# Optimization experiments

Measured on AMD Instinct MI355X. Metric: run time of the kernel, lower is better.

The kernel has to match this reference:

```python
import jax, jax.numpy as jnp
import numpy as np
import math

B, T, C = 2, 2048, 2048
H, G, HS = 16, 4, 128  # n_head, n_query_groups, head_size
EPS = 1e-5
SCALE = 1.0 / math.sqrt(HS)
QKV_DIM = (H + 2 * G) * HS  # 3072, gate logits (H) appended after


def _build_rope(seq_len, n_elem, base):
    freq = base ** (np.arange(0, n_elem, 2, dtype=np.float64) / n_elem)
    inv_freq = 1.0 / freq
    idx_theta = np.outer(np.arange(seq_len, dtype=np.float64), inv_freq)
    return (jnp.asarray(np.cos(idx_theta), dtype=jnp.float32),
            jnp.asarray(np.sin(idx_theta), dtype=jnp.float32))


def setup_inputs() -> dict:
    key = jax.random.key(0)
    k1, k2, k3 = jax.random.split(key, 3)
    x = jax.random.normal(k1, (B, T, C), dtype=jnp.float32)
    # rope base per module: 0.09 * local_window ** 1.628
    base = 0.09 * (2048.0 ** 1.628)
    cos, sin = _build_rope(T, HS, base)  # [T, HS//2]
    W_attn = jax.random.normal(k2, (QKV_DIM + H, C), dtype=jnp.float32) * 0.02
    W_proj = jax.random.normal(k3, (C, H * HS), dtype=jnp.float32) * 0.02
    q_norm_w = jnp.ones((HS,), dtype=jnp.float32)
    k_norm_w = jnp.ones((HS,), dtype=jnp.float32)
    return {"x": x, "cos": cos, "sin": sin, "W_attn": W_attn,
            "q_norm_w": q_norm_w, "k_norm_w": k_norm_w, "W_proj": W_proj}


def _rms_norm(v, w):
    # per-head RMSNorm over last dim (head_size)
    ms = jnp.mean(jnp.square(v), axis=-1, keepdims=True)
    return v * jax.lax.rsqrt(ms + EPS) * w


def _apply_rope(v, cos, sin):
    # v: [B, T, N, HS]; cos/sin: [T, HS//2]; non-interleaved halves
    d2 = v.shape[-1] // 2
    x1, x2 = v[..., :d2], v[..., d2:]
    c = cos[None, :, None, :]
    s = sin[None, :, None, :]
    return jnp.concatenate([x1 * c - x2 * s, x2 * c + x1 * s], axis=-1)


def reference(x, cos, sin, W_attn, q_norm_w, k_norm_w, W_proj):
    qkv = jnp.einsum('btc,oc->bto', x, W_attn)  # [B, T, QKV_DIM+H]
    q = qkv[..., : H * HS].reshape(B, T, H, HS)
    k = qkv[..., H * HS:(H + G) * HS].reshape(B, T, G, HS)
    v = qkv[..., (H + G) * HS: QKV_DIM].reshape(B, T, G, HS)
    gate = qkv[..., QKV_DIM:]  # [B, T, H]

    q = _apply_rope(_rms_norm(q, q_norm_w), cos, sin)
    k = _apply_rope(_rms_norm(k, k_norm_w), cos, sin)

    rep = H // G
    kr = jnp.repeat(k, rep, axis=2)  # [B, T, H, HS]
    vr = jnp.repeat(v, rep, axis=2)

    scores = jnp.einsum('bthd,bshd->bhts', q, kr) * SCALE  # [B, H, T, T]
    causal = jnp.tril(jnp.ones((T, T), dtype=bool))
    scores = jnp.where(causal, scores, jnp.finfo(scores.dtype).min)
    probs = jax.nn.softmax(scores, axis=-1)
    out = jnp.einsum('bhts,bshd->bthd', probs, vr)  # [B, T, H, HS]

    out = out * jax.nn.sigmoid(gate)[..., None]  # gated attention, per-head
    y = jnp.einsum('bto,co->btc', out.reshape(B, T, H * HS), W_proj)
    return y
```

## Files before the change

### kernel.cpp

```cpp
#include <hip/hip_runtime.h>

#define T_   2048
#define BB   2
#define CC   2048
#define HH   16
#define GG   4
#define HSS  128
#define QKVD 3072
#define NQKV 3088
#define NPAD 3200
#define SCALE_ 0.08838834764831845f
#define SCALE2_ (0.08838834764831845f * 1.4426950408889634f)

typedef __attribute__((ext_vector_type(8))) short  short8;
typedef __attribute__((ext_vector_type(4))) float  f32x4;
typedef __attribute__((ext_vector_type(4))) int    v4i;
typedef __attribute__((ext_vector_type(4))) float  v4f;
typedef __attribute__((ext_vector_type(4))) unsigned short u16x4;

typedef const void __attribute__((address_space(1)))* gas1_t;
typedef void __attribute__((address_space(3)))* as3_t;

__device__ __forceinline__ void gl_lds16(const void* g, void* l) {
    __builtin_amdgcn_global_load_lds((gas1_t)g, (as3_t)l, 16, 0, 0);
}

__device__ __forceinline__ unsigned short f2bf(float f) {
    unsigned u = __float_as_uint(f);
    u += 0x7fffu + ((u >> 16) & 1u);
    return (unsigned short)(u >> 16);
}
__device__ __forceinline__ unsigned short f2bf_fast(float f) {
    return (unsigned short)((__float_as_uint(f) + 0x8000u) >> 16);
}
__device__ __forceinline__ float bf2f(unsigned short h) {
    return __uint_as_float(((unsigned)h) << 16);
}

template <int CTRL>
__device__ __forceinline__ float dppmv(float x) {
    int i = __float_as_int(x);
    return __int_as_float(__builtin_amdgcn_update_dpp(i, i, CTRL, 0xF, 0xF, false));
}
__device__ __forceinline__ void red16_max(float* v) {
#pragma unroll
    for (int r = 0; r < 4; ++r) v[r] = fmaxf(v[r], dppmv<0xB1>(v[r]));
#pragma unroll
    for (int r = 0; r < 4; ++r) v[r] = fmaxf(v[r], dppmv<0x4E>(v[r]));
#pragma unroll
    for (int r = 0; r < 4; ++r) v[r] = fmaxf(v[r], dppmv<0x124>(v[r]));
#pragma unroll
    for (int r = 0; r < 4; ++r) v[r] = fmaxf(v[r], dppmv<0x128>(v[r]));
}
__device__ __forceinline__ void red16_sum(float* v) {
#pragma unroll
    for (int r = 0; r < 4; ++r) v[r] += dppmv<0xB1>(v[r]);
#pragma unroll
    for (int r = 0; r < 4; ++r) v[r] += dppmv<0x4E>(v[r]);
#pragma unroll
    for (int r = 0; r < 4; ++r) v[r] += dppmv<0x124>(v[r]);
#pragma unroll
    for (int r = 0; r < 4; ++r) v[r] += dppmv<0x128>(v[r]);
}

__global__ void k_convert3(const float* __restrict__ x, const float* __restrict__ wa,
                           const float* __restrict__ wp,
                           unsigned short* __restrict__ xb, unsigned short* __restrict__ wab,
                           unsigned short* __restrict__ wpb) {
    const int id = blockIdx.x;
    const float* src; unsigned short* dst; int base, n_src4;
    if (id < 8192)       { src = x;  dst = xb;  base = id;         n_src4 = 2097152; }
    else if (id < 14592) { src = wa; dst = wab; base = id - 8192;  n_src4 = 1581056; }
    else                 { src = wp; dst = wpb; base = id - 14592; n_src4 = 1048576; }
    int i = base * 256 + threadIdx.x;
    u16x4 o;
    if (i < n_src4) {
        v4f v = *(const v4f*)(src + (size_t)i * 4);
        o[0] = f2bf(v[0]); o[1] = f2bf(v[1]); o[2] = f2bf(v[2]); o[3] = f2bf(v[3]);
    } else {
        o[0] = 0; o[1] = 0; o[2] = 0; o[3] = 0;
    }
    *(u16x4*)(dst + (size_t)i * 4) = o;
}

template <int BM_, typename OutT>
__launch_bounds__(512, 2)
__global__ void k_gemm8(const unsigned short* __restrict__ A,
                        const unsigned short* __restrict__ Bm,
                        OutT* __restrict__ C,
                        int K, int lda, int ldb, int ldc, int nmax) {
    constexpr int MI  = BM_ / 32;
    constexpr int NPH = MI / 2;
    __shared__ unsigned short As[2][BM_ * 64];
    __shared__ unsigned short Bs[2][256 * 64];
    const int t = threadIdx.x;
    const int lane = t & 63;
    const int wid  = t >> 6;
    const int wr = wid >> 2, wc = wid & 3;
    const int bm = blockIdx.x, bn = blockIdx.y;
    const int fro = lane & 15, fk = lane >> 4;

    const int srow  = lane >> 3;
    const size_t scol = (size_t)(((lane & 7) ^ srow) * 8);

    const unsigned short* Abase = A  + (size_t)(bm * BM_) * lda;
    const unsigned short* Bbase = Bm + (size_t)(bn * 256) * ldb;

    f32x4 acc[MI][4];
#pragma unroll
    for (int i = 0; i < MI; ++i)
#pragma unroll
        for (int j = 0; j < 4; ++j) acc[i][j] = (f32x4){0.f, 0.f, 0.f, 0.f};

#pragma unroll
    for (int h = 0; h < 2; ++h)
#pragma unroll
        for (int c8 = 0; c8 < 2; ++c8) {
            const int rr = h * 128 + wid * 16 + c8 * 8;
            if (BM_ == 256 || h == 0)
                gl_lds16(Abase + (size_t)(rr + srow) * lda + scol, &As[0][rr * 64]);
            gl_lds16(Bbase + (size_t)(rr + srow) * ldb + scol, &Bs[0][rr * 64]);
        }

    int cur = 0;
    for (int kt = 0; kt < K; kt += 64) {
        asm volatile("s_waitcnt vmcnt(0)" ::: "memory");
        __builtin_amdgcn_s_barrier();
        __builtin_amdgcn_sched_barrier(0);
        const bool pf = (kt + 64 < K);
        const int nxt = cur ^ 1;
        const int kn = kt + 64;

        short8 bf_[4][2];
#pragma unroll
        for (int q = 0; q < NPH; ++q) {
            short8 af[2][2];
#pragma unroll
            for (int im = 0; im < 2; ++im)
#pragma unroll
                for (int kk = 0; kk < 2; ++kk) {
                    const int ar = wr * (BM_ / 2) + (q * 2 + im) * 16 + fro;
                    af[im][kk] = *(const short8*)&As[cur][ar * 64 + ((kk * 4 + fk) ^ (ar & 7)) * 8];
                }
            if (q == 0) {
#pragma unroll
                for (int ni = 0; ni < 4; ++ni)
#pragma unroll
                    for (int kk = 0; kk < 2; ++kk) {
                        const int br = wc * 64 + ni * 16 + fro;
                        bf_[ni][kk] = *(const short8*)&Bs[cur][br * 64 + ((kk * 4 + fk) ^ (br & 7)) * 8];
                    }
            }
            if (pf) {
                if (BM_ == 256) {
                    const int h = q & 1;
#pragma unroll
                    for (int c8 = 0; c8 < 2; ++c8) {
                        const int rr = h * 128 + wid * 16 + c8 * 8;
                        if ((q >> 1) == 0)
                            gl_lds16(Abase + (size_t)(rr + srow) * lda + kn + scol, &As[nxt][rr * 64]);
                        else
                            gl_lds16(Bbase + (size_t)(rr + srow) * ldb + kn + scol, &Bs[nxt][rr * 64]);
                    }
                } else {
                    if (q == 0) {
#pragma unroll
                        for (int c8 = 0; c8 < 2; ++c8) {
                            const int rr = wid * 16 + c8 * 8;
                            gl_lds16(Abase + (size_t)(rr + srow) * lda + kn + scol, &As[nxt][rr * 64]);
                        }
                    } else {
#pragma unroll
                        for (int h = 0; h < 2; ++h)
#pragma unroll
                            for (int c8 = 0; c8 < 2; ++c8) {
                                const int rr = h * 128 + wid * 16 + c8 * 8;
                                gl_lds16(Bbase + (size_t)(rr + srow) * ldb + kn + scol, &Bs[nxt][rr * 64]);
                            }
                    }
                }
            }
            __builtin_amdgcn_s_setprio(1);
#pragma unroll
            for (int im = 0; im < 2; ++im)
#pragma unroll
                for (int ni = 0; ni < 4; ++ni)
#pragma unroll
                    for (int kk = 0; kk < 2; ++kk)
                        acc[q * 2 + im][ni] = __builtin_amdgcn_mfma_f32_16x16x32_bf16(
                            af[im][kk], bf_[ni][kk], acc[q * 2 + im][ni], 0, 0, 0);
            __builtin_amdgcn_s_setprio(0);
            __builtin_amdgcn_s_barrier();
        }
        cur ^= 1;
    }

    const int col16 = lane & 15, rbase = (lane >> 4) * 4;
    const int gr0 = bm * BM_ + wr * (BM_ / 2);
    const int gc0 = bn * 256 + wc * 64;
#pragma unroll
    for (int mi = 0; mi < MI; ++mi)
#pragma unroll
        for (int ni = 0; ni < 4; ++ni) {
            const int gcol = gc0 + ni * 16 + col16;
            if (gcol < nmax) {
#pragma unroll
                for (int r = 0; r < 4; ++r) {
                    const int grow = gr0 + mi * 16 + rbase + r;
                    float v = acc[mi][ni][r];
                    if constexpr (sizeof(OutT) == 2)
                        C[(size_t)grow * ldc + gcol] = (OutT)f2bf(v);
                    else
                        C[(size_t)grow * ldc + gcol] = (OutT)v;
                }
            }
        }
}

__global__ void k_normtrans(unsigned short* __restrict__ qkv,
                            const float* __restrict__ cosT, const float* __restrict__ sinT,
                            const float* __restrict__ qw, const float* __restrict__ kw,
                            unsigned short* __restrict__ vt) {
    __shared__ unsigned short tile[64][65];
    const int id = blockIdx.x;
    if (id < 20480) {
        const int lane = threadIdx.x & 63;
        const int row  = id * 4 + (threadIdx.x >> 6);
        const int tok  = row / 20;
        const int hh   = row - tok * 20;
        const int tpos = tok & (T_ - 1);
        unsigned short* rp = qkv + (size_t)tok * NPAD + (hh < 16 ? hh * 128 : 2048 + (hh - 16) * 128);
        const float* w = (hh < 16) ? qw : kw;
        const float sc_ = (hh < 16) ? SCALE2_ : 1.0f;
        float e1 = bf2f(rp[lane]);
        float e2 = bf2f(rp[lane + 64]);
        float ss = e1 * e1 + e2 * e2;
#pragma unroll
        for (int m = 1; m < 64; m <<= 1) ss += __shfl_xor(ss, m);
        float inv = rsqrtf(ss * (1.0f / 128.0f) + 1e-5f);
        float n1 = e1 * inv * w[lane];
        float n2 = e2 * inv * w[lane + 64];
        float c = cosT[tpos * 64 + lane];
        float s = sinT[tpos * 64 + lane];
        rp[lane]      = f2bf((n1 * c - n2 * s) * sc_);
        rp[lane + 64] = f2bf((n2 * c + n1 * s) * sc_);
    } else {
        const int t2 = id - 20480;
        const int b = (t2 & 7) >> 2, g = t2 & 3;
        const int s0 = ((t2 >> 3) & 31) * 64, d0 = (t2 >> 8) * 64;
        const int tx = threadIdx.x & 63, ty0 = threadIdx.x >> 6;
        const unsigned short* src = qkv + (size_t)(b * T_ + s0) * NPAD + 2560 + g * 128 + d0;
#pragma unroll
        for (int r = 0; r < 16; ++r) {
            int ty = ty0 * 16 + r;
            tile[ty][tx] = src[(size_t)ty * NPAD + tx];
        }
        __syncthreads();
        unsigned short* dstp = vt + ((size_t)(b * GG + g) * 128 + d0) * T_ + s0;
#pragma unroll
        for (int r = 0; r < 16; ++r) {
            int ty = ty0 * 16 + r;
            dstp[(size_t)ty * T_ + tx] = tile[tx][ty];
        }
    }
}

__launch_bounds__(512, 4)
__global__ void k_attn(const unsigned short* __restrict__ qkv,
                       const unsigned short* __restrict__ vt,
                       unsigned short* __restrict__ ao) {
    __shared__ unsigned short Ks[64 * 128];
    __shared__ unsigned short Vs[128 * 64];
    __shared__ unsigned short Ps[8][16 * 64];
    const int t = threadIdx.x;
    const int lane = t & 63;
    const int wid  = t >> 6;
    const int id = blockIdx.x;
    const int bg = id & 7;
    const int hh = (id >> 3) & 3;
    const int prx = (id >> 5) & 7;
    const int pr = (id & 256) ? (15 - prx) : prx;
    const int b = bg >> 2, g = bg & 3, h = g * 4 + hh;
    const int fro = lane & 15, fk = lane >> 4;
    const int rbase = fk * 4;

    const int qt  = (wid < 4) ? pr : 31 - pr;
    const int wq  = wid & 3;
    const int q0w = qt * 64 + wq * 16;
    const int nt_own  = qt + 1;
    const int nt_loop = 32 - pr;

    const unsigned short* kg0 = qkv + (size_t)(b * T_) * NPAD + 2048 + g * 128;
    const unsigned short* vg0 = vt + (size_t)(b * GG + g) * 128 * T_;

    short8 qf[4];
    const unsigned short* qp = qkv + (size_t)(b * T_ + q0w + fro) * NPAD + h * 128 + fk * 8;
#pragma unroll
    for (int kb = 0; kb < 4; ++kb) qf[kb] = *(const short8*)(qp + kb * 32);

    float m_r[4], l_r[4];
    f32x4 o[8];
#pragma unroll
    for (int r = 0; r < 4; ++r) { m_r[r] = -1e30f; l_r[r] = 0.f; }
#pragma unroll
    for (int d = 0; d < 8; ++d) o[d] = (f32x4){0.f, 0.f, 0.f, 0.f};

    const int cp0 = wid * 2;

    for (int ti = 0; ti < nt_loop; ++ti) {
        const int s0 = ti * 64;
        __syncthreads();
#pragma unroll
        for (int p = 0; p < 2; ++p) {
            const int cp = cp0 + p;
            const int kr = cp * 4 + (lane >> 4);
            const int sK = lane & 15;
            gl_lds16(kg0 + (size_t)(s0 + kr) * NPAD + (size_t)((sK ^ (kr & 7)) * 8), &Ks[cp * 512]);
            const int d  = cp * 8 + (lane >> 3);
            const int sV = lane & 7;
            gl_lds16(vg0 + (size_t)d * T_ + s0 + (size_t)((sV ^ (d & 7)) * 8), &Vs[cp * 512]);
        }
        __syncthreads();

        if (ti < nt_own) {
            f32x4 sc[4];
#pragma unroll
            for (int jb = 0; jb < 4; ++jb) sc[jb] = (f32x4){0.f, 0.f, 0.f, 0.f};
#pragma unroll
            for (int jb = 0; jb < 4; ++jb) {
                const int kr = jb * 16 + fro;
#pragma unroll
                for (int kb = 0; kb < 4; ++kb) {
                    short8 kf = *(const short8*)&Ks[kr * 128 + 8 * ((kb * 4 + fk) ^ (kr & 7))];
                    sc[jb] = __builtin_amdgcn_mfma_f32_16x16x32_bf16(qf[kb], kf, sc[jb], 0, 0, 0);
                }
            }
            if (ti == qt) {
#pragma unroll
                for (int jb = 0; jb < 4; ++jb)
#pragma unroll
                    for (int r = 0; r < 4; ++r)
                        if ((jb * 16 + fro) > (wq * 16 + rbase + r)) sc[jb][r] = -1e30f;
            }
            float mx[4], rs[4];
#pragma unroll
            for (int r = 0; r < 4; ++r)
                mx[r] = fmaxf(fmaxf(sc[0][r], sc[1][r]), fmaxf(sc[2][r], sc[3][r]));
            red16_max(mx);
            bool grow = false;
#pragma unroll
            for (int r = 0; r < 4; ++r) grow = grow || (mx[r] > m_r[r] + 8.f);
            if (__any(grow ? 1 : 0)) {
#pragma unroll
                for (int r = 0; r < 4; ++r) {
                    float mn = fmaxf(m_r[r], mx[r]);
                    float fs = exp2f(m_r[r] - mn);
                    m_r[r] = mn;
                    l_r[r] *= fs;
#pragma unroll
                    for (int d = 0; d < 8; ++d) o[d][r] *= fs;
                }
            }
#pragma unroll
            for (int jb = 0; jb < 4; ++jb)
#pragma unroll
                for (int r = 0; r < 4; ++r) sc[jb][r] = exp2f(sc[jb][r] - m_r[r]);
#pragma unroll
            for (int r = 0; r < 4; ++r)
                rs[r] = (sc[0][r] + sc[1][r]) + (sc[2][r] + sc[3][r]);
            red16_sum(rs);
#pragma unroll
            for (int r = 0; r < 4; ++r) l_r[r] += rs[r];
            unsigned short* pw = &Ps[wid][0];
#pragma unroll
            for (int jb = 0; jb < 4; ++jb)
#pragma unroll
                for (int r = 0; r < 4; ++r) {
                    const int row = rbase + r;
                    const int slot = jb * 2 + (fro >> 3);
                    pw[row * 64 + ((slot ^ (row & 7)) * 8 + (fro & 7))] = f2bf_fast(sc[jb][r]);
                }
            asm volatile("s_waitcnt lgkmcnt(0)" ::: "memory");
            __builtin_amdgcn_sched_barrier(0);
            short8 pa[2];
#pragma unroll
            for (int ks = 0; ks < 2; ++ks)
                pa[ks] = *(const short8*)&Ps[wid][fro * 64 + ((ks * 4 + fk) ^ (fro & 7)) * 8];
#pragma unroll
            for (int ks = 0; ks < 2; ++ks)
#pragma unroll
                for (int db = 0; db < 8; ++db) {
                    const int d = db * 16 + fro;
                    short8 vf = *(const short8*)&Vs[d * 64 + 8 * ((ks * 4 + fk) ^ (d & 7))];
                    o[db] = __builtin_amdgcn_mfma_f32_16x16x32_bf16(pa[ks], vf, o[db], 0, 0, 0);
                }
        }
    }
#pragma unroll
    for (int r = 0; r < 4; ++r) {
        const int qrow = q0w + rbase + r;
        float gv = bf2f(qkv[(size_t)(b * T_ + qrow) * NPAD + QKVD + h]);
        float sg = 1.f / (1.f + __expf(-gv));
        float invl = sg / l_r[r];
        unsigned short* orow = ao + (size_t)(b * T_ + qrow) * 2048 + h * 128;
#pragma unroll
        for (int db = 0; db < 8; ++db)
            orow[db * 16 + fro] = f2bf(o[db][r] * invl);
    }
}

extern "C" void kernel_launch(void* const* d_in, const int* in_sizes, int n_in,
                              void* d_out, int out_size, void* d_ws, size_t ws_size,
                              hipStream_t stream) {
    const float* x      = (const float*)d_in[0];
    const float* cosT   = (const float*)d_in[1];
    const float* sinT   = (const float*)d_in[2];
    const float* W_attn = (const float*)d_in[3];
    const float* qw     = (const float*)d_in[4];
    const float* kw     = (const float*)d_in[5];
    const float* W_proj = (const float*)d_in[6];

    char* ws = (char*)d_ws;
    const size_t OFF_XB   = 0;
    const size_t OFF_WAB  = 16777216;
    const size_t OFF_WPB  = 29884416;
    const size_t OFF_QKV  = 38273024;
    const size_t OFF_VT   = 64487424;
    const size_t OFF_AO   = 68681728;
    const size_t NEED     = 85458944;
    if (ws_size < NEED) return;

    unsigned short* xb   = (unsigned short*)(ws + OFF_XB);
    unsigned short* wab  = (unsigned short*)(ws + OFF_WAB);
    unsigned short* wpb  = (unsigned short*)(ws + OFF_WPB);
    unsigned short* qkvb = (unsigned short*)(ws + OFF_QKV);
    unsigned short* vtb  = (unsigned short*)(ws + OFF_VT);
    unsigned short* aob  = (unsigned short*)(ws + OFF_AO);

    k_convert3<<<18688, 256, 0, stream>>>(x, W_attn, W_proj, xb, wab, wpb);
    k_gemm8<256, unsigned short><<<dim3(16, 13), 512, 0, stream>>>(xb, wab, qkvb, 2048, 2048, 2048, NPAD, NPAD);
    k_normtrans<<<20992, 256, 0, stream>>>(qkvb, cosT, sinT, qw, kw, vtb);
    k_attn<<<512, 512, 0, stream>>>(qkvb, vtb, aob);
    k_gemm8<128, float><<<dim3(32, 8), 512, 0, stream>>>(aob, wpb, (float*)d_out, 2048, 2048, 2048, 2048, 2048);
}
```

Baseline: 211.2 us.

## Split long causal query tile across both wave groups with split-K merge

Reworks the attention work split so that, once the short query tile finishes, wave group A takes half of the KV range of the long query tile while group B handles the other half. The two partial softmax states are merged through LDS before the gated epilogue. This balances per-wave work inside each block, so the short-tile waves no longer sit idle at barriers while the long tile runs. The cost is a second K/V LDS buffer (raising LDS use, which may limit occupancy), extra staging traffic per iteration and a merge step at the end.

Result: slower. 221.6 us (+4.9%).

```diff
diff --git a/kernel.cpp b/kernel.cpp
--- a/kernel.cpp
+++ b/kernel.cpp
@@ -269,8 +269,10 @@
 __global__ void k_attn(const unsigned short* __restrict__ qkv,
                        const unsigned short* __restrict__ vt,
                        unsigned short* __restrict__ ao) {
-    __shared__ unsigned short Ks[64 * 128];
-    __shared__ unsigned short Vs[128 * 64];
+    __shared__ unsigned short KsB[64 * 128];
+    __shared__ unsigned short VsB[128 * 64];
+    __shared__ unsigned short KsA[64 * 128];
+    __shared__ unsigned short VsA[128 * 64];
     __shared__ unsigned short Ps[8][16 * 64];
     const int t = threadIdx.x;
     const int lane = t & 63;
@@ -283,20 +285,13 @@
     const int b = bg >> 2, g = bg & 3, h = g * 4 + hh;
     const int fro = lane & 15, fk = lane >> 4;
     const int rbase = fk * 4;
-
-    const int qt  = (wid < 4) ? pr : 31 - pr;
-    const int wq  = wid & 3;
-    const int q0w = qt * 64 + wq * 16;
-    const int nt_own  = qt + 1;
-    const int nt_loop = 32 - pr;
+    const bool grpA = (wid < 4);
+    const int wq = wid & 3;
+    const int qtB = 31 - pr;
 
     const unsigned short* kg0 = qkv + (size_t)(b * T_) * NPAD + 2048 + g * 128;
     const unsigned short* vg0 = vt + (size_t)(b * GG + g) * 128 * T_;
-
-    short8 qf[4];
-    const unsigned short* qp = qkv + (size_t)(b * T_ + q0w + fro) * NPAD + h * 128 + fk * 8;
-#pragma unroll
-    for (int kb = 0; kb < 4; ++kb) qf[kb] = *(const short8*)(qp + kb * 32);
+    const int cp0 = wid * 2;
 
     float m_r[4], l_r[4];
     f32x4 o[8];
@@ -305,107 +300,176 @@
 #pragma unroll
     for (int d = 0; d < 8; ++d) o[d] = (f32x4){0.f, 0.f, 0.f, 0.f};
 
-    const int cp0 = wid * 2;
-
-    for (int ti = 0; ti < nt_loop; ++ti) {
-        const int s0 = ti * 64;
-        __syncthreads();
+    short8 qf[4];
+    {
+        const int q0 = (grpA ? pr : qtB) * 64 + wq * 16;
+        const unsigned short* qp = qkv + (size_t)(b * T_ + q0 + fro) * NPAD + h * 128 + fk * 8;
+#pragma unroll
+        for (int kb = 0; kb < 4; ++kb) qf[kb] = *(const short8*)(qp + kb * 32);
+    }
+
+    auto stage_pair = [&](unsigned short* Kd, unsigned short* Vd, int tile) {
+        const int s0 = tile * 64;
 #pragma unroll
         for (int p = 0; p < 2; ++p) {
             const int cp = cp0 + p;
             const int kr = cp * 4 + (lane >> 4);
             const int sK = lane & 15;
-            gl_lds16(kg0 + (size_t)(s0 + kr) * NPAD + (size_t)((sK ^ (kr & 7)) * 8), &Ks[cp * 512]);
+            gl_lds16(kg0 + (size_t)(s0 + kr) * NPAD + (size_t)((sK ^ (kr & 7)) * 8), &Kd[cp * 512]);
             const int d  = cp * 8 + (lane >> 3);
             const int sV = lane & 7;
-            gl_lds16(vg0 + (size_t)d * T_ + s0 + (size_t)((sV ^ (d & 7)) * 8), &Vs[cp * 512]);
-        }
+            gl_lds16(vg0 + (size_t)d * T_ + s0 + (size_t)((sV ^ (d & 7)) * 8), &Vd[cp * 512]);
+        }
+    };
+
+    auto compute_tile = [&](const unsigned short* Kb, const unsigned short* Vb, bool domask) {
+        f32x4 sc[4];
+#pragma unroll
+        for (int jb = 0; jb < 4; ++jb) sc[jb] = (f32x4){0.f, 0.f, 0.f, 0.f};
+#pragma unroll
+        for (int jb = 0; jb < 4; ++jb) {
+            const int kr = jb * 16 + fro;
+#pragma unroll
+            for (int kb = 0; kb < 4; ++kb) {
+                short8 kf = *(const short8*)&Kb[kr * 128 + 8 * ((kb * 4 + fk) ^ (kr & 7))];
+                sc[jb] = __builtin_amdgcn_mfma_f32_16x16x32_bf16(qf[kb], kf, sc[jb], 0, 0, 0);
+            }
+        }
+        if (domask) {
+#pragma unroll
+            for (int jb = 0; jb < 4; ++jb)
+#pragma unroll
+                for (int r = 0; r < 4; ++r)
+                    if ((jb * 16 + fro) > (wq * 16 + rbase + r)) sc[jb][r] = -1e30f;
+        }
+        float mx[4], rs[4];
+#pragma unroll
+        for (int r = 0; r < 4; ++r)
+            mx[r] = fmaxf(fmaxf(sc[0][r], sc[1][r]), fmaxf(sc[2][r], sc[3][r]));
+        red16_max(mx);
+        bool growb = false;
+#pragma unroll
+        for (int r = 0; r < 4; ++r) growb = growb || (mx[r] > m_r[r] + 8.f);
+        if (__any(growb ? 1 : 0)) {
+#pragma unroll
+            for (int r = 0; r < 4; ++r) {
+                float mn = fmaxf(m_r[r], mx[r]);
+                float fs = exp2f(m_r[r] - mn);
+                m_r[r] = mn;
+                l_r[r] *= fs;
+#pragma unroll
+                for (int d = 0; d < 8; ++d) o[d][r] *= fs;
+            }
+        }
+#pragma unroll
+        for (int jb = 0; jb < 4; ++jb)
+#pragma unroll
+            for (int r = 0; r < 4; ++r) sc[jb][r] = exp2f(sc[jb][r] - m_r[r]);
+#pragma unroll
+        for (int r = 0; r < 4; ++r)
+            rs[r] = (sc[0][r] + sc[1][r]) + (sc[2][r] + sc[3][r]);
+        red16_sum(rs);
+#pragma unroll
+        for (int r = 0; r < 4; ++r) l_r[r] += rs[r];
+        unsigned short* pw = &Ps[wid][0];
+#pragma unroll
+        for (int jb = 0; jb < 4; ++jb)
+#pragma unroll
+            for (int r = 0; r < 4; ++r) {
+                const int row = rbase + r;
+                const int slot = jb * 2 + (fro >> 3);
+                pw[row * 64 + ((slot ^ (row & 7)) * 8 + (fro & 7))] = f2bf_fast(sc[jb][r]);
+            }
+        asm volatile("s_waitcnt lgkmcnt(0)" ::: "memory");
+        __builtin_amdgcn_sched_barrier(0);
+        short8 pa[2];
+#pragma unroll
+        for (int ks = 0; ks < 2; ++ks)
+            pa[ks] = *(const short8*)&Ps[wid][fro * 64 + ((ks * 4 + fk) ^ (fro & 7)) * 8];
+#pragma unroll
+        for (int ks = 0; ks < 2; ++ks)
+#pragma unroll
+            for (int db = 0; db < 8; ++db) {
+                const int d = db * 16 + fro;
+                short8 vf = *(const short8*)&Vb[d * 64 + 8 * ((ks * 4 + fk) ^ (d & 7))];
+                o[db] = __builtin_amdgcn_mfma_f32_16x16x32_bf16(pa[ks], vf, o[db], 0, 0, 0);
+            }
+    };
+
+    auto epilogue = [&](int q0e) {
+#pragma unroll
+        for (int r = 0; r < 4; ++r) {
+            const int qrow = q0e + rbase + r;
+            float gv = bf2f(qkv[(size_t)(b * T_ + qrow) * NPAD + QKVD + h]);
+            float sg = 1.f / (1.f + __expf(-gv));
+            float invl = sg / l_r[r];
+            unsigned short* orow = ao + (size_t)(b * T_ + qrow) * 2048 + h * 128;
+#pragma unroll
+            for (int db = 0; db < 8; ++db)
+                orow[db * 16 + fro] = f2bf(o[db][r] * invl);
+        }
+    };
+
+    for (int s = 0; s <= pr; ++s) {
         __syncthreads();
-
-        if (ti < nt_own) {
-            f32x4 sc[4];
-#pragma unroll
-            for (int jb = 0; jb < 4; ++jb) sc[jb] = (f32x4){0.f, 0.f, 0.f, 0.f};
-#pragma unroll
-            for (int jb = 0; jb < 4; ++jb) {
-                const int kr = jb * 16 + fro;
-#pragma unroll
-                for (int kb = 0; kb < 4; ++kb) {
-                    short8 kf = *(const short8*)&Ks[kr * 128 + 8 * ((kb * 4 + fk) ^ (kr & 7))];
-                    sc[jb] = __builtin_amdgcn_mfma_f32_16x16x32_bf16(qf[kb], kf, sc[jb], 0, 0, 0);
-                }
-            }
-            if (ti == qt) {
-#pragma unroll
-                for (int jb = 0; jb < 4; ++jb)
-#pragma unroll
-                    for (int r = 0; r < 4; ++r)
-                        if ((jb * 16 + fro) > (wq * 16 + rbase + r)) sc[jb][r] = -1e30f;
-            }
-            float mx[4], rs[4];
-#pragma unroll
-            for (int r = 0; r < 4; ++r)
-                mx[r] = fmaxf(fmaxf(sc[0][r], sc[1][r]), fmaxf(sc[2][r], sc[3][r]));
-            red16_max(mx);
-            bool grow = false;
-#pragma unroll
-            for (int r = 0; r < 4; ++r) grow = grow || (mx[r] > m_r[r] + 8.f);
-            if (__any(grow ? 1 : 0)) {
-#pragma unroll
-                for (int r = 0; r < 4; ++r) {
-                    float mn = fmaxf(m_r[r], mx[r]);
-                    float fs = exp2f(m_r[r] - mn);
-                    m_r[r] = mn;
-                    l_r[r] *= fs;
-#pragma unroll
-                    for (int d = 0; d < 8; ++d) o[d][r] *= fs;
-                }
-            }
-#pragma unroll
-            for (int jb = 0; jb < 4; ++jb)
-#pragma unroll
-                for (int r = 0; r < 4; ++r) sc[jb][r] = exp2f(sc[jb][r] - m_r[r]);
-#pragma unroll
-            for (int r = 0; r < 4; ++r)
-                rs[r] = (sc[0][r] + sc[1][r]) + (sc[2][r] + sc[3][r]);
-            red16_sum(rs);
-#pragma unroll
-            for (int r = 0; r < 4; ++r) l_r[r] += rs[r];
-            unsigned short* pw = &Ps[wid][0];
-#pragma unroll
-            for (int jb = 0; jb < 4; ++jb)
-#pragma unroll
-                for (int r = 0; r < 4; ++r) {
-                    const int row = rbase + r;
-                    const int slot = jb * 2 + (fro >> 3);
-                    pw[row * 64 + ((slot ^ (row & 7)) * 8 + (fro & 7))] = f2bf_fast(sc[jb][r]);
-                }
-            asm volatile("s_waitcnt lgkmcnt(0)" ::: "memory");
-            __builtin_amdgcn_sched_barrier(0);
-            short8 pa[2];
-#pragma unroll
-            for (int ks = 0; ks < 2; ++ks)
-                pa[ks] = *(const short8*)&Ps[wid][fro * 64 + ((ks * 4 + fk) ^ (fro & 7)) * 8];
-#pragma unroll
-            for (int ks = 0; ks < 2; ++ks)
-#pragma unroll
-                for (int db = 0; db < 8; ++db) {
-                    const int d = db * 16 + fro;
-                    short8 vf = *(const short8*)&Vs[d * 64 + 8 * ((ks * 4 + fk) ^ (d & 7))];
-                    o[db] = __builtin_amdgcn_mfma_f32_16x16x32_bf16(pa[ks], vf, o[db], 0, 0, 0);
-                }
-        }
-    }
-#pragma unroll
-    for (int r = 0; r < 4; ++r) {
-        const int qrow = q0w + rbase + r;
-        float gv = bf2f(qkv[(size_t)(b * T_ + qrow) * NPAD + QKVD + h]);
-        float sg = 1.f / (1.f + __expf(-gv));
-        float invl = sg / l_r[r];
-        unsigned short* orow = ao + (size_t)(b * T_ + qrow) * 2048 + h * 128;
-#pragma unroll
-        for (int db = 0; db < 8; ++db)
-            orow[db * 16 + fro] = f2bf(o[db][r] * invl);
+        stage_pair(KsB, VsB, s);
+        __syncthreads();
+        compute_tile(KsB, VsB, grpA && (s == pr));
+    }
+
+    if (grpA) {
+        epilogue(pr * 64 + wq * 16);
+#pragma unroll
+        for (int r = 0; r < 4; ++r) { m_r[r] = -1e30f; l_r[r] = 0.f; }
+#pragma unroll
+        for (int d = 0; d < 8; ++d) o[d] = (f32x4){0.f, 0.f, 0.f, 0.f};
+        const int q0 = qtB * 64 + wq * 16;
+        const unsigned short* qp = qkv + (size_t)(b * T_ + q0 + fro) * NPAD + h * 128 + fk * 8;
+#pragma unroll
+        for (int kb = 0; kb < 4; ++kb) qf[kb] = *(const short8*)(qp + kb * 32);
+    }
+
+    for (int s = pr + 1; s <= 16; ++s) {
+        __syncthreads();
+        stage_pair(KsB, VsB, s);
+        if (s <= 15) stage_pair(KsA, VsA, s + 16 - pr);
+        __syncthreads();
+        if (!grpA)
+            compute_tile(KsB, VsB, (s == 16) && (pr == 15));
+        else if (s <= 15)
+            compute_tile(KsA, VsA, (s == 15) && (pr < 15));
+    }
+
+    __syncthreads();
+    const int ww = wid & 3;
+    unsigned short* obase = (ww & 2) ? VsB : KsB;
+    float* ob = (float*)(obase + (ww & 1) * 4096);
+    float* ml = (float*)KsA + ww * 512;
+    if (grpA) {
+#pragma unroll
+        for (int d = 0; d < 8; ++d) *(f32x4*)&ob[lane * 32 + d * 4] = o[d];
+#pragma unroll
+        for (int r = 0; r < 4; ++r) { ml[lane * 8 + r] = m_r[r]; ml[lane * 8 + 4 + r] = l_r[r]; }
+    }
+    __syncthreads();
+    if (!grpA) {
+        float sB[4], sA[4];
+#pragma unroll
+        for (int r = 0; r < 4; ++r) {
+            float mA = ml[lane * 8 + r];
+            float lA = ml[lane * 8 + 4 + r];
+            float mn = fmaxf(m_r[r], mA);
+            sB[r] = exp2f(m_r[r] - mn);
+            sA[r] = exp2f(mA - mn);
+            l_r[r] = l_r[r] * sB[r] + lA * sA[r];
+        }
+#pragma unroll
+        for (int d = 0; d < 8; ++d) {
+            f32x4 oA = *(const f32x4*)&ob[lane * 32 + d * 4];
+#pragma unroll
+            for (int r = 0; r < 4; ++r) o[d][r] = o[d][r] * sB[r] + oA[r] * sA[r];
+        }
+        epilogue(qtB * 64 + wq * 16);
     }
 }
 
```

## Give each attention wave 32 query rows so K/V fragments feed two MFMAs

Applied to the files above, without the earlier changes.

The attention kernel now runs 4 waves (256 threads) per block instead of 8, and each wave owns 32 query rows as two 16-row sub-tiles. Each K and V fragment read from LDS feeds two MFMAs, which halves LDS read traffic per FLOP and halves the per-block wave count. In exchange, each wave needs roughly twice the registers for accumulators and softmax state. The launch bounds drop to 3 blocks per CU, so fewer waves are resident to hide latency.

New measurement: 315.7 us. 49.4% more time.

```diff
diff --git a/kernel.cpp b/kernel.cpp
--- a/kernel.cpp
+++ b/kernel.cpp
@@ -42,25 +42,27 @@
     int i = __float_as_int(x);
     return __int_as_float(__builtin_amdgcn_update_dpp(i, i, CTRL, 0xF, 0xF, false));
 }
-__device__ __forceinline__ void red16_max(float* v) {
-#pragma unroll
-    for (int r = 0; r < 4; ++r) v[r] = fmaxf(v[r], dppmv<0xB1>(v[r]));
-#pragma unroll
-    for (int r = 0; r < 4; ++r) v[r] = fmaxf(v[r], dppmv<0x4E>(v[r]));
-#pragma unroll
-    for (int r = 0; r < 4; ++r) v[r] = fmaxf(v[r], dppmv<0x124>(v[r]));
-#pragma unroll
-    for (int r = 0; r < 4; ++r) v[r] = fmaxf(v[r], dppmv<0x128>(v[r]));
-}
-__device__ __forceinline__ void red16_sum(float* v) {
-#pragma unroll
-    for (int r = 0; r < 4; ++r) v[r] += dppmv<0xB1>(v[r]);
-#pragma unroll
-    for (int r = 0; r < 4; ++r) v[r] += dppmv<0x4E>(v[r]);
-#pragma unroll
-    for (int r = 0; r < 4; ++r) v[r] += dppmv<0x124>(v[r]);
-#pragma unroll
-    for (int r = 0; r < 4; ++r) v[r] += dppmv<0x128>(v[r]);
+template <int N>
+__device__ __forceinline__ void red16_maxN(float* v) {
+#pragma unroll
+    for (int r = 0; r < N; ++r) v[r] = fmaxf(v[r], dppmv<0xB1>(v[r]));
+#pragma unroll
+    for (int r = 0; r < N; ++r) v[r] = fmaxf(v[r], dppmv<0x4E>(v[r]));
+#pragma unroll
+    for (int r = 0; r < N; ++r) v[r] = fmaxf(v[r], dppmv<0x124>(v[r]));
+#pragma unroll
+    for (int r = 0; r < N; ++r) v[r] = fmaxf(v[r], dppmv<0x128>(v[r]));
+}
+template <int N>
+__device__ __forceinline__ void red16_sumN(float* v) {
+#pragma unroll
+    for (int r = 0; r < N; ++r) v[r] += dppmv<0xB1>(v[r]);
+#pragma unroll
+    for (int r = 0; r < N; ++r) v[r] += dppmv<0x4E>(v[r]);
+#pragma unroll
+    for (int r = 0; r < N; ++r) v[r] += dppmv<0x124>(v[r]);
+#pragma unroll
+    for (int r = 0; r < N; ++r) v[r] += dppmv<0x128>(v[r]);
 }
 
 __global__ void k_convert3(const float* __restrict__ x, const float* __restrict__ wa,
@@ -265,13 +267,13 @@
     }
 }
 
-__launch_bounds__(512, 4)
+__launch_bounds__(256, 3)
 __global__ void k_attn(const unsigned short* __restrict__ qkv,
                        const unsigned short* __restrict__ vt,
                        unsigned short* __restrict__ ao) {
     __shared__ unsigned short Ks[64 * 128];
     __shared__ unsigned short Vs[128 * 64];
-    __shared__ unsigned short Ps[8][16 * 64];
+    __shared__ unsigned short Ps[4][32 * 64];
     const int t = threadIdx.x;
     const int lane = t & 63;
     const int wid  = t >> 6;
@@ -284,34 +286,42 @@
     const int fro = lane & 15, fk = lane >> 4;
     const int rbase = fk * 4;
 
-    const int qt  = (wid < 4) ? pr : 31 - pr;
-    const int wq  = wid & 3;
-    const int q0w = qt * 64 + wq * 16;
+    const bool grpA = (wid < 2);
+    const int wq2 = wid & 1;
+    const int qt  = grpA ? pr : 31 - pr;
+    const int q0w = qt * 64 + wq2 * 32;
     const int nt_own  = qt + 1;
     const int nt_loop = 32 - pr;
 
     const unsigned short* kg0 = qkv + (size_t)(b * T_) * NPAD + 2048 + g * 128;
     const unsigned short* vg0 = vt + (size_t)(b * GG + g) * 128 * T_;
 
-    short8 qf[4];
-    const unsigned short* qp = qkv + (size_t)(b * T_ + q0w + fro) * NPAD + h * 128 + fk * 8;
-#pragma unroll
-    for (int kb = 0; kb < 4; ++kb) qf[kb] = *(const short8*)(qp + kb * 32);
-
-    float m_r[4], l_r[4];
-    f32x4 o[8];
-#pragma unroll
-    for (int r = 0; r < 4; ++r) { m_r[r] = -1e30f; l_r[r] = 0.f; }
-#pragma unroll
-    for (int d = 0; d < 8; ++d) o[d] = (f32x4){0.f, 0.f, 0.f, 0.f};
-
-    const int cp0 = wid * 2;
+    short8 qf[2][4];
+#pragma unroll
+    for (int i = 0; i < 2; ++i) {
+        const unsigned short* qp = qkv + (size_t)(b * T_ + q0w + i * 16 + fro) * NPAD + h * 128 + fk * 8;
+#pragma unroll
+        for (int kb = 0; kb < 4; ++kb) qf[i][kb] = *(const short8*)(qp + kb * 32);
+    }
+
+    float m_r[2][4], l_r[2][4];
+    f32x4 o[2][8];
+#pragma unroll
+    for (int i = 0; i < 2; ++i)
+#pragma unroll
+        for (int r = 0; r < 4; ++r) { m_r[i][r] = -1e30f; l_r[i][r] = 0.f; }
+#pragma unroll
+    for (int i = 0; i < 2; ++i)
+#pragma unroll
+        for (int d = 0; d < 8; ++d) o[i][d] = (f32x4){0.f, 0.f, 0.f, 0.f};
+
+    const int cp0 = wid * 4;
 
     for (int ti = 0; ti < nt_loop; ++ti) {
         const int s0 = ti * 64;
         __syncthreads();
 #pragma unroll
-        for (int p = 0; p < 2; ++p) {
+        for (int p = 0; p < 4; ++p) {
             const int cp = cp0 + p;
             const int kr = cp * 4 + (lane >> 4);
             const int sK = lane & 15;
@@ -323,90 +333,116 @@
         __syncthreads();
 
         if (ti < nt_own) {
-            f32x4 sc[4];
-#pragma unroll
-            for (int jb = 0; jb < 4; ++jb) sc[jb] = (f32x4){0.f, 0.f, 0.f, 0.f};
+            f32x4 sc[2][4];
+#pragma unroll
+            for (int i = 0; i < 2; ++i)
+#pragma unroll
+                for (int jb = 0; jb < 4; ++jb) sc[i][jb] = (f32x4){0.f, 0.f, 0.f, 0.f};
 #pragma unroll
             for (int jb = 0; jb < 4; ++jb) {
                 const int kr = jb * 16 + fro;
 #pragma unroll
                 for (int kb = 0; kb < 4; ++kb) {
                     short8 kf = *(const short8*)&Ks[kr * 128 + 8 * ((kb * 4 + fk) ^ (kr & 7))];
-                    sc[jb] = __builtin_amdgcn_mfma_f32_16x16x32_bf16(qf[kb], kf, sc[jb], 0, 0, 0);
+#pragma unroll
+                    for (int i = 0; i < 2; ++i)
+                        sc[i][jb] = __builtin_amdgcn_mfma_f32_16x16x32_bf16(qf[i][kb], kf, sc[i][jb], 0, 0, 0);
                 }
             }
             if (ti == qt) {
 #pragma unroll
+                for (int i = 0; i < 2; ++i)
+#pragma unroll
+                    for (int jb = 0; jb < 4; ++jb)
+#pragma unroll
+                        for (int r = 0; r < 4; ++r)
+                            if ((jb * 16 + fro) > (wq2 * 32 + i * 16 + rbase + r)) sc[i][jb][r] = -1e30f;
+            }
+            float mx[8], rs[8];
+#pragma unroll
+            for (int i = 0; i < 2; ++i)
+#pragma unroll
+                for (int r = 0; r < 4; ++r)
+                    mx[i * 4 + r] = fmaxf(fmaxf(sc[i][0][r], sc[i][1][r]), fmaxf(sc[i][2][r], sc[i][3][r]));
+            red16_maxN<8>(mx);
+            bool grow = false;
+#pragma unroll
+            for (int i = 0; i < 2; ++i)
+#pragma unroll
+                for (int r = 0; r < 4; ++r) grow = grow || (mx[i * 4 + r] > m_r[i][r] + 8.f);
+            if (__any(grow ? 1 : 0)) {
+#pragma unroll
+                for (int i = 0; i < 2; ++i)
+#pragma unroll
+                    for (int r = 0; r < 4; ++r) {
+                        float mn = fmaxf(m_r[i][r], mx[i * 4 + r]);
+                        float fs = exp2f(m_r[i][r] - mn);
+                        m_r[i][r] = mn;
+                        l_r[i][r] *= fs;
+#pragma unroll
+                        for (int d = 0; d < 8; ++d) o[i][d][r] *= fs;
+                    }
+            }
+#pragma unroll
+            for (int i = 0; i < 2; ++i)
+#pragma unroll
                 for (int jb = 0; jb < 4; ++jb)
 #pragma unroll
-                    for (int r = 0; r < 4; ++r)
-                        if ((jb * 16 + fro) > (wq * 16 + rbase + r)) sc[jb][r] = -1e30f;
-            }
-            float mx[4], rs[4];
-#pragma unroll
-            for (int r = 0; r < 4; ++r)
-                mx[r] = fmaxf(fmaxf(sc[0][r], sc[1][r]), fmaxf(sc[2][r], sc[3][r]));
-            red16_max(mx);
-            bool grow = false;
-#pragma unroll
-            for (int r = 0; r < 4; ++r) grow = grow || (mx[r] > m_r[r] + 8.f);
-            if (__any(grow ? 1 : 0)) {
-#pragma unroll
-                for (int r = 0; r < 4; ++r) {
-                    float mn = fmaxf(m_r[r], mx[r]);
-                    float fs = exp2f(m_r[r] - mn);
-                    m_r[r] = mn;
-                    l_r[r] *= fs;
-#pragma unroll
-                    for (int d = 0; d < 8; ++d) o[d][r] *= fs;
-                }
-            }
-#pragma unroll
-            for (int jb = 0; jb < 4; ++jb)
-#pragma unroll
-                for (int r = 0; r < 4; ++r) sc[jb][r] = exp2f(sc[jb][r] - m_r[r]);
-#pragma unroll
-            for (int r = 0; r < 4; ++r)
-                rs[r] = (sc[0][r] + sc[1][r]) + (sc[2][r] + sc[3][r]);
-            red16_sum(rs);
-#pragma unroll
-            for (int r = 0; r < 4; ++r) l_r[r] += rs[r];
+                    for (int r = 0; r < 4; ++r) sc[i][jb][r] = exp2f(sc[i][jb][r] - m_r[i][r]);
+#pragma unroll
+            for (int i = 0; i < 2; ++i)
+#pragma unroll
+                for (int r = 0; r < 4; ++r)
+                    rs[i * 4 + r] = (sc[i][0][r] + sc[i][1][r]) + (sc[i][2][r] + sc[i][3][r]);
+            red16_sumN<8>(rs);
+#pragma unroll
+            for (int i = 0; i < 2; ++i)
+#pragma unroll
+                for (int r = 0; r < 4; ++r) l_r[i][r] += rs[i * 4 + r];
             unsigned short* pw = &Ps[wid][0];
 #pragma unroll
-            for (int jb = 0; jb < 4; ++jb)
-#pragma unroll
-                for (int r = 0; r < 4; ++r) {
-                    const int row = rbase + r;
-                    const int slot = jb * 2 + (fro >> 3);
-                    pw[row * 64 + ((slot ^ (row & 7)) * 8 + (fro & 7))] = f2bf_fast(sc[jb][r]);
-                }
+            for (int i = 0; i < 2; ++i)
+#pragma unroll
+                for (int jb = 0; jb < 4; ++jb)
+#pragma unroll
+                    for (int r = 0; r < 4; ++r) {
+                        const int row = i * 16 + rbase + r;
+                        const int slot = jb * 2 + (fro >> 3);
+                        pw[row * 64 + ((slot ^ (row & 7)) * 8 + (fro & 7))] = f2bf_fast(sc[i][jb][r]);
+                    }
             asm volatile("s_waitcnt lgkmcnt(0)" ::: "memory");
             __builtin_amdgcn_sched_barrier(0);
-            short8 pa[2];
-#pragma unroll
-            for (int ks = 0; ks < 2; ++ks)
-                pa[ks] = *(const short8*)&Ps[wid][fro * 64 + ((ks * 4 + fk) ^ (fro & 7)) * 8];
+            short8 pa[2][2];
+#pragma unroll
+            for (int i = 0; i < 2; ++i)
+#pragma unroll
+                for (int ks = 0; ks < 2; ++ks)
+                    pa[i][ks] = *(const short8*)&Ps[wid][(i * 16 + fro) * 64 + ((ks * 4 + fk) ^ (fro & 7)) * 8];
 #pragma unroll
             for (int ks = 0; ks < 2; ++ks)
 #pragma unroll
                 for (int db = 0; db < 8; ++db) {
                     const int d = db * 16 + fro;
                     short8 vf = *(const short8*)&Vs[d * 64 + 8 * ((ks * 4 + fk) ^ (d & 7))];
-                    o[db] = __builtin_amdgcn_mfma_f32_16x16x32_bf16(pa[ks], vf, o[db], 0, 0, 0);
+#pragma unroll
+                    for (int i = 0; i < 2; ++i)
+                        o[i][db] = __builtin_amdgcn_mfma_f32_16x16x32_bf16(pa[i][ks], vf, o[i][db], 0, 0, 0);
                 }
         }
     }
 #pragma unroll
-    for (int r = 0; r < 4; ++r) {
-        const int qrow = q0w + rbase + r;
-        float gv = bf2f(qkv[(size_t)(b * T_ + qrow) * NPAD + QKVD + h]);
-        float sg = 1.f / (1.f + __expf(-gv));
-        float invl = sg / l_r[r];
-        unsigned short* orow = ao + (size_t)(b * T_ + qrow) * 2048 + h * 128;
-#pragma unroll
-        for (int db = 0; db < 8; ++db)
-            orow[db * 16 + fro] = f2bf(o[db][r] * invl);
-    }
+    for (int i = 0; i < 2; ++i)
+#pragma unroll
+        for (int r = 0; r < 4; ++r) {
+            const int qrow = q0w + i * 16 + rbase + r;
+            float gv = bf2f(qkv[(size_t)(b * T_ + qrow) * NPAD + QKVD + h]);
+            float sg = 1.f / (1.f + __expf(-gv));
+            float invl = sg / l_r[i][r];
+            unsigned short* orow = ao + (size_t)(b * T_ + qrow) * 2048 + h * 128;
+#pragma unroll
+            for (int db = 0; db < 8; ++db)
+                orow[db * 16 + fro] = f2bf(o[i][db][r] * invl);
+        }
 }
 
 extern "C" void kernel_launch(void* const* d_in, const int* in_sizes, int n_in,
@@ -440,6 +476,6 @@
     k_convert3<<<18688, 256, 0, stream>>>(x, W_attn, W_proj, xb, wab, wpb);
     k_gemm8<256, unsigned short><<<dim3(16, 13), 512, 0, stream>>>(xb, wab, qkvb, 2048, 2048, 2048, NPAD, NPAD);
     k_normtrans<<<20992, 256, 0, stream>>>(qkvb, cosT, sinT, qw, kw, vtb);
-    k_attn<<<512, 512, 0, stream>>>(qkvb, vtb, aob);
+    k_attn<<<512, 256, 0, stream>>>(qkvb, vtb, aob);
     k_gemm8<128, float><<<dim3(32, 8), 512, 0, stream>>>(aob, wpb, (float*)d_out, 2048, 2048, 2048, 2048, 2048);
 }
```
